# Kernel tuning notes

Hardware: AMD Instinct MI355X
Metric: run time of the kernel (lower is better)

The kernel has to match this reference:

```python
import jax, jax.numpy as jnp
import numpy as np

B, N, F, H, OUT = 64, 512, 128, 256, 6


def setup_inputs() -> dict:
    key = jax.random.key(0)
    ks = jax.random.split(key, 20)
    s = 0.02
    inp = {
        "x": jax.random.normal(ks[0], (B * N, F), dtype=jnp.float32),
        "edge_index": jax.random.randint(ks[1], (2, 16), 0, B * N),
        "edge_weight": jax.random.uniform(ks[2], (16,), dtype=jnp.float32),
        "batch": jnp.repeat(jnp.arange(B, dtype=jnp.int64), N),
        "sigma": jax.random.uniform(ks[3], (1,), dtype=jnp.float32),
        "Wg": s * jax.random.normal(ks[4], (F, F)), "bg": jnp.zeros((F,)),
        "Wrel0": s * jax.random.normal(ks[5], (F, H)), "Wroot0": s * jax.random.normal(ks[6], (F, H)), "brel0": jnp.zeros((H,)),
        "Wrel1": s * jax.random.normal(ks[7], (H, H)), "Wroot1": s * jax.random.normal(ks[8], (H, H)), "brel1": jnp.zeros((H,)),
        "Wrel2": s * jax.random.normal(ks[9], (H, H)), "Wroot2": s * jax.random.normal(ks[10], (H, H)), "brel2": jnp.zeros((H,)),
        "W1": s * jax.random.normal(ks[11], (H, H)), "b1": jnp.zeros((H,)),
        "Wout": s * jax.random.normal(ks[12], (H, OUT)), "bout": jnp.zeros((OUT,)),
    }
    return inp


def _forward(x, sigma, Wg, bg, Wrel0, Wroot0, brel0, Wrel1, Wroot1, brel1,
             Wrel2, Wroot2, brel2, W1, b1, Wout, bout):
    # gdmLinear
    h = x @ Wg + bg                      # [B*N, F]
    hw = h.reshape(B, N, -1)             # to_dense_batch (equal-size windows)
    # pairwise squared distances per window -> Gaussian kernel
    sq = jnp.sum(hw * hw, axis=-1)       # [B, N]
    dist = jnp.maximum(sq[:, :, None] + sq[:, None, :]
                       - 2.0 * jnp.einsum('bnf,bmf->bnm', hw, hw), 0.0)
    A = jnp.exp(-dist / (2.0 * sigma[0] ** 2))   # [B, N, N], all > 0
    A = A * (1.0 - jnp.eye(N, dtype=A.dtype))    # nonzero extraction drops self-loops

    def conv(h, Wrel, Wroot, brel):
        # GraphConv: out_i = W_rel @ sum_j A[j,i] * h_j + b_rel + W_root @ h_i
        agg = jnp.einsum('bji,bjf->bif', A, h)
        return agg @ Wrel + brel + h @ Wroot

    h = hw
    h = jax.nn.relu(conv(h, Wrel0, Wroot0, brel0))
    h = jax.nn.relu(conv(h, Wrel1, Wroot1, brel1))
    h = conv(h, Wrel2, Wroot2, brel2)
    g = jnp.mean(h, axis=1)              # global_mean_pool (equal-size graphs)
    g = jax.nn.relu(g @ W1 + b1)
    return g @ Wout + bout               # [B, OUT]


def reference(x, edge_index, edge_weight, batch, sigma, Wg, bg,
              Wrel0, Wroot0, brel0, Wrel1, Wroot1, brel1,
              Wrel2, Wroot2, brel2, W1, b1, Wout, bout):
    # edge_index / edge_weight / batch inputs are recomputed internally by GdmGNN
    return _forward(x, sigma, Wg, bg, Wrel0, Wroot0, brel0, Wrel1, Wroot1, brel1,
                    Wrel2, Wroot2, brel2, W1, b1, Wout, bout)
```

## Files before the change

kernel.cpp:

```cpp
#include <hip/hip_runtime.h>
#include <math.h>

#define Bsz 64
#define Nn 512
#define Ff 128
#define Hh 256
#define OUTD 6
#define MTOT (Bsz * Nn)

typedef __bf16 bf16x8 __attribute__((ext_vector_type(8)));
typedef float f32x4 __attribute__((ext_vector_type(4)));
typedef int int4v __attribute__((ext_vector_type(4)));
typedef unsigned short ushort4v __attribute__((ext_vector_type(4)));

__device__ __forceinline__ unsigned short f2bf(float f) {
    unsigned u = __float_as_uint(f);
    u += 0x7FFFu + ((u >> 16) & 1u);
    return (unsigned short)(u >> 16);
}
__device__ __forceinline__ float bf2f(unsigned short s) {
    return __uint_as_float(((unsigned)s) << 16);
}

#define SWZ(r) (((r) ^ ((r) >> 2)) & 3)

__device__ __forceinline__ void async_ld16(const unsigned short* g, unsigned short* l) {
    __builtin_amdgcn_global_load_lds(
        (const __attribute__((address_space(1))) void*)g,
        (__attribute__((address_space(3))) void*)l,
        16, 0, 0);
}

#define LDH 40
#define TSZ (128 * 32)
#define AGP 136
#define AGP1 264

__global__ __launch_bounds__(512) void fused_l0(
    const unsigned short* __restrict__ h0T,
    const unsigned short* __restrict__ Arows,
    const unsigned short* __restrict__ h0b,
    const unsigned short* __restrict__ WrelT0,
    const unsigned short* __restrict__ WrootT0,
    const float* __restrict__ brel0,
    unsigned short* __restrict__ h1b,
    unsigned short* __restrict__ h1T)
{
    int id = blockIdx.x;
    int b = id & 63;
    int nt = id >> 6;
    int n0g = nt * 128;
    long nodeBase = (long)b * Nn + n0g;

    const unsigned short* HT = h0T + (long)b * Ff * Nn;
    const unsigned short* AR = Arows + (long)b * Nn * Nn;

    __shared__ unsigned short SA[2 * TSZ];
    __shared__ unsigned short SB[2 * TSZ];
    __shared__ unsigned short aggL[128 * AGP];

    int tid = threadIdx.x;
    int lane = tid & 63;
    int wave = tid >> 6;
    int quad = lane >> 4, l16 = lane & 15;
    int wm = (wave >> 1) * 32, wn = (wave & 1) * 64;
    int sr = lane >> 2, sc = lane & 3;

    {
        f32x4 acc[2][4] = {};
        auto issue = [&](int g) {
            int kk = g << 5;
            unsigned short* Ad = SA + (g & 1) * TSZ;
            unsigned short* Bd = SB + (g & 1) * TSZ;
            int r = wave * 16 + sr;
            int c = sc ^ SWZ(r);
            async_ld16(HT + (long)r * Nn + kk + c * 8, Ad + (wave * 16) * 32);
            async_ld16(AR + (long)(n0g + r) * Nn + kk + c * 8, Bd + (wave * 16) * 32);
        };
        issue(0);
        for (int g = 0; g < (Nn >> 5); ++g) {
            __syncthreads();
            if (g + 1 < (Nn >> 5)) issue(g + 1);
            const unsigned short* Ab = SA + (g & 1) * TSZ;
            const unsigned short* Bb = SB + (g & 1) * TSZ;
            bf16x8 af[2], bfr[4];
            #pragma unroll
            for (int i = 0; i < 2; ++i) {
                int r = wm + i * 16 + l16;
                af[i] = *(const bf16x8*)&Ab[r * 32 + (quad ^ SWZ(r)) * 8];
            }
            #pragma unroll
            for (int j = 0; j < 4; ++j) {
                int r = wn + j * 16 + l16;
                bfr[j] = *(const bf16x8*)&Bb[r * 32 + (quad ^ SWZ(r)) * 8];
            }
            #pragma unroll
            for (int i = 0; i < 2; ++i)
                #pragma unroll
                for (int j = 0; j < 4; ++j)
                    acc[i][j] = __builtin_amdgcn_mfma_f32_16x16x32_bf16(
                        af[i], bfr[j], acc[i][j], 0, 0, 0);
        }
        #pragma unroll
        for (int i = 0; i < 2; ++i) {
            int f = wm + i * 16 + quad * 4;
            #pragma unroll
            for (int j = 0; j < 4; ++j) {
                int nl = wn + j * 16 + l16;
                f32x4 v = acc[i][j];
                ushort4v p;
                p[0] = f2bf(v[0]); p[1] = f2bf(v[1]);
                p[2] = f2bf(v[2]); p[3] = f2bf(v[3]);
                *(ushort4v*)&aggL[nl * AGP + f] = p;
            }
        }
    }
    __syncthreads();

    for (int half = 0; half < 2; ++half) {
        int m0 = half * 128;
        f32x4 acc[2][4] = {};
        auto issue = [&](int g) {
            unsigned short* Ad = SA + (g & 1) * TSZ;
            int r = wave * 16 + sr;
            int c = sc ^ SWZ(r);
            if (g < 4) {
                async_ld16(WrelT0 + (long)(m0 + r) * Ff + (g << 5) + c * 8,
                           Ad + (wave * 16) * 32);
            } else {
                async_ld16(WrootT0 + (long)(m0 + r) * Ff + ((g - 4) << 5) + c * 8,
                           Ad + (wave * 16) * 32);
                unsigned short* Bd = SB + (g & 1) * TSZ;
                async_ld16(h0b + (nodeBase + r) * Ff + ((g - 4) << 5) + c * 8,
                           Bd + (wave * 16) * 32);
            }
        };
        issue(0);
        for (int g = 0; g < 8; ++g) {
            __syncthreads();
            if (g + 1 < 8) issue(g + 1);
            const unsigned short* Ab = SA + (g & 1) * TSZ;
            bf16x8 af[2], bfr[4];
            #pragma unroll
            for (int i = 0; i < 2; ++i) {
                int r = wm + i * 16 + l16;
                af[i] = *(const bf16x8*)&Ab[r * 32 + (quad ^ SWZ(r)) * 8];
            }
            if (g < 4) {
                #pragma unroll
                for (int j = 0; j < 4; ++j) {
                    int nl = wn + j * 16 + l16;
                    bfr[j] = *(const bf16x8*)&aggL[nl * AGP + (g << 5) + quad * 8];
                }
            } else {
                const unsigned short* Bb = SB + (g & 1) * TSZ;
                #pragma unroll
                for (int j = 0; j < 4; ++j) {
                    int r = wn + j * 16 + l16;
                    bfr[j] = *(const bf16x8*)&Bb[r * 32 + (quad ^ SWZ(r)) * 8];
                }
            }
            #pragma unroll
            for (int i = 0; i < 2; ++i)
                #pragma unroll
                for (int j = 0; j < 4; ++j)
                    acc[i][j] = __builtin_amdgcn_mfma_f32_16x16x32_bf16(
                        af[i], bfr[j], acc[i][j], 0, 0, 0);
        }
        #pragma unroll
        for (int i = 0; i < 2; ++i) {
            int of = m0 + wm + i * 16 + quad * 4;
            float b0 = brel0[of + 0], b1 = brel0[of + 1];
            float b2 = brel0[of + 2], b3 = brel0[of + 3];
            #pragma unroll
            for (int j = 0; j < 4; ++j) {
                int nl = wn + j * 16 + l16;
                f32x4 v = acc[i][j];
                float o0 = fmaxf(v[0] + b0, 0.f), o1 = fmaxf(v[1] + b1, 0.f);
                float o2 = fmaxf(v[2] + b2, 0.f), o3 = fmaxf(v[3] + b3, 0.f);
                ushort4v p;
                p[0] = f2bf(o0); p[1] = f2bf(o1); p[2] = f2bf(o2); p[3] = f2bf(o3);
                *(ushort4v*)&h1b[(nodeBase + nl) * Hh + of] = p;
                long base = ((long)b * Hh) * 512 + n0g + nl;
                h1T[base + (long)(of + 0) * 512] = p[0];
                h1T[base + (long)(of + 1) * 512] = p[1];
                h1T[base + (long)(of + 2) * 512] = p[2];
                h1T[base + (long)(of + 3) * 512] = p[3];
            }
        }
    }
}

__global__ __launch_bounds__(512) void fused_l1(
    const unsigned short* __restrict__ h1T,
    const unsigned short* __restrict__ Arows,
    const unsigned short* __restrict__ h1b,
    const unsigned short* __restrict__ WrelT1,
    const unsigned short* __restrict__ WrootT1,
    const float* __restrict__ brel1,
    const float* __restrict__ w,
    float* __restrict__ vpart, float* __restrict__ mpart)
{
    constexpr int ATS = 256 * 32;
    constexpr int BTS = 64 * 32;

    int id = blockIdx.x;
    int b = id & 63;
    int nt = id >> 6;
    int n0g = nt * 64;
    long nodeBase = (long)b * Nn + n0g;

    const unsigned short* HT = h1T + (long)b * Hh * Nn;
    const unsigned short* AR = Arows + (long)b * Nn * Nn;

    __shared__ unsigned short SA[2 * ATS];
    __shared__ unsigned short SB[2 * BTS];
    __shared__ unsigned short aggL[64 * AGP1];

    int tid = threadIdx.x;
    int lane = tid & 63;
    int wave = tid >> 6;
    int quad = lane >> 4, l16 = lane & 15;
    int wm = wave * 32;
    int sr = lane >> 2, sc = lane & 3;

    {
        f32x4 acc[2][4] = {};
        auto issue = [&](int g) {
            int kk = g << 5;
            unsigned short* Ad = SA + (g & 1) * ATS;
            int r = wave * 16 + sr;
            int c = sc ^ SWZ(r);
            async_ld16(HT + (long)r * Nn + kk + c * 8, Ad + (wave * 16) * 32);
            int r2 = 128 + r;
            int c2 = sc ^ SWZ(r2);
            async_ld16(HT + (long)r2 * Nn + kk + c2 * 8, Ad + (128 + wave * 16) * 32);
            if (wave < 4) {
                unsigned short* Bd = SB + (g & 1) * BTS;
                async_ld16(AR + (long)(n0g + r) * Nn + kk + c * 8,
                           Bd + (wave * 16) * 32);
            }
        };
        issue(0);
        for (int g = 0; g < 16; ++g) {
            __syncthreads();
            if (g + 1 < 16) issue(g + 1);
            const unsigned short* Ab = SA + (g & 1) * ATS;
            const unsigned short* Bb = SB + (g & 1) * BTS;
            bf16x8 af[2], bfr[4];
            #pragma unroll
            for (int i = 0; i < 2; ++i) {
                int r = wm + i * 16 + l16;
                af[i] = *(const bf16x8*)&Ab[r * 32 + (quad ^ SWZ(r)) * 8];
            }
            #pragma unroll
            for (int j = 0; j < 4; ++j) {
                int r = j * 16 + l16;
                bfr[j] = *(const bf16x8*)&Bb[r * 32 + (quad ^ SWZ(r)) * 8];
            }
            #pragma unroll
            for (int i = 0; i < 2; ++i)
                #pragma unroll
                for (int j = 0; j < 4; ++j)
                    acc[i][j] = __builtin_amdgcn_mfma_f32_16x16x32_bf16(
                        af[i], bfr[j], acc[i][j], 0, 0, 0);
        }
        #pragma unroll
        for (int i = 0; i < 2; ++i) {
            int f = wm + i * 16 + quad * 4;
            #pragma unroll
            for (int j = 0; j < 4; ++j) {
                int nl = j * 16 + l16;
                f32x4 v = acc[i][j];
                ushort4v p;
                p[0] = f2bf(v[0]); p[1] = f2bf(v[1]);
                p[2] = f2bf(v[2]); p[3] = f2bf(v[3]);
                *(ushort4v*)&aggL[nl * AGP1 + f] = p;
            }
        }
    }
    __syncthreads();

    f32x4 acc[2][4] = {};
    auto issue2 = [&](int g) {
        const unsigned short* Wp = (g < 8) ? WrelT1 : WrootT1;
        int kk = (g & 7) << 5;
        unsigned short* Ad = SA + (g & 1) * ATS;
        int r = wave * 16 + sr;
        int c = sc ^ SWZ(r);
        async_ld16(Wp + (long)r * Hh + kk + c * 8, Ad + (wave * 16) * 32);
        int r2 = 128 + r;
        int c2 = sc ^ SWZ(r2);
        async_ld16(Wp + (long)r2 * Hh + kk + c2 * 8, Ad + (128 + wave * 16) * 32);
        if (g >= 8 && wave < 4) {
            unsigned short* Bd = SB + (g & 1) * BTS;
            async_ld16(h1b + (nodeBase + r) * Hh + kk + c * 8, Bd + (wave * 16) * 32);
        }
    };
    issue2(0);
    for (int g = 0; g < 16; ++g) {
        __syncthreads();
        if (g + 1 < 16) issue2(g + 1);
        const unsigned short* Ab = SA + (g & 1) * ATS;
        bf16x8 af[2], bfr[4];
        #pragma unroll
        for (int i = 0; i < 2; ++i) {
            int r = wm + i * 16 + l16;
            af[i] = *(const bf16x8*)&Ab[r * 32 + (quad ^ SWZ(r)) * 8];
        }
        if (g < 8) {
            #pragma unroll
            for (int j = 0; j < 4; ++j) {
                int nl = j * 16 + l16;
                bfr[j] = *(const bf16x8*)&aggL[nl * AGP1 + (g << 5) + quad * 8];
            }
        } else {
            const unsigned short* Bb = SB + (g & 1) * BTS;
            #pragma unroll
            for (int j = 0; j < 4; ++j) {
                int r = j * 16 + l16;
                bfr[j] = *(const bf16x8*)&Bb[r * 32 + (quad ^ SWZ(r)) * 8];
            }
        }
        #pragma unroll
        for (int i = 0; i < 2; ++i)
            #pragma unroll
            for (int j = 0; j < 4; ++j)
                acc[i][j] = __builtin_amdgcn_mfma_f32_16x16x32_bf16(
                    af[i], bfr[j], acc[i][j], 0, 0, 0);
    }

    #pragma unroll
    for (int i = 0; i < 2; ++i) {
        int lf = wm + i * 16 + quad * 4;
        float b0 = brel1[lf + 0], b1 = brel1[lf + 1];
        float b2 = brel1[lf + 2], b3 = brel1[lf + 3];
        float vp0 = 0.f, vp1 = 0.f, vp2 = 0.f, vp3 = 0.f;
        float mp0 = 0.f, mp1 = 0.f, mp2 = 0.f, mp3 = 0.f;
        #pragma unroll
        for (int j = 0; j < 4; ++j) {
            long node = nodeBase + j * 16 + l16;
            f32x4 v = acc[i][j];
            float o0 = fmaxf(v[0] + b0, 0.f), o1 = fmaxf(v[1] + b1, 0.f);
            float o2 = fmaxf(v[2] + b2, 0.f), o3 = fmaxf(v[3] + b3, 0.f);
            float h0v = bf2f(f2bf(o0)), h1v = bf2f(f2bf(o1));
            float h2v = bf2f(f2bf(o2)), h3v = bf2f(f2bf(o3));
            float wv = w[node];
            vp0 += wv * h0v; vp1 += wv * h1v; vp2 += wv * h2v; vp3 += wv * h3v;
            mp0 += h0v; mp1 += h1v; mp2 += h2v; mp3 += h3v;
        }
        #pragma unroll
        for (int m = 1; m < 16; m <<= 1) {
            vp0 += __shfl_xor(vp0, m); vp1 += __shfl_xor(vp1, m);
            vp2 += __shfl_xor(vp2, m); vp3 += __shfl_xor(vp3, m);
            mp0 += __shfl_xor(mp0, m); mp1 += __shfl_xor(mp1, m);
            mp2 += __shfl_xor(mp2, m); mp3 += __shfl_xor(mp3, m);
        }
        if (l16 == 0) {
            long o = ((long)(b * 8 + nt)) * Hh + lf;
            float4 vv = {vp0, vp1, vp2, vp3};
            float4 mm = {mp0, mp1, mp2, mp3};
            *(float4*)&vpart[o] = vv;
            *(float4*)&mpart[o] = mm;
        }
    }
}

__global__ __launch_bounds__(256) void prep_h0(
    const float* __restrict__ x, const float* __restrict__ Wg,
    const float* __restrict__ bg,
    const float* __restrict__ Wrel0, const float* __restrict__ Wroot0,
    const float* __restrict__ Wrel1, const float* __restrict__ Wroot1,
    unsigned short* __restrict__ T0, unsigned short* __restrict__ T1,
    unsigned short* __restrict__ T2, unsigned short* __restrict__ T3,
    float* __restrict__ w,
    unsigned short* __restrict__ h0b, unsigned short* __restrict__ h0T,
    float* __restrict__ sqv)
{
    if (blockIdx.x < 896) {
        int idx = blockIdx.x * 256 + threadIdx.x;
        if (idx >= 196608) { w[idx - 196608] = 0.f; return; }
        const float* src; unsigned short* dst; int kin; int e;
        if      (idx <  32768) { src = Wrel0;  dst = T0; kin = 128; e = idx; }
        else if (idx <  65536) { src = Wroot0; dst = T1; kin = 128; e = idx - 32768; }
        else if (idx < 131072) { src = Wrel1;  dst = T2; kin = 256; e = idx - 65536; }
        else                   { src = Wroot1; dst = T3; kin = 256; e = idx - 131072; }
        int o = (kin == 128) ? (e >> 7) : (e >> 8);
        int i = e & (kin - 1);
        dst[e] = f2bf(src[(long)i * 256 + o]);
        return;
    }

    __shared__ unsigned short As[128 * LDH];
    __shared__ unsigned short Bs[128 * LDH];
    __shared__ float rsq[128];

    int tid = threadIdx.x;
    int lane = tid & 63;
    int wave = tid >> 6;
    int quad = lane >> 4, l16 = lane & 15;
    int wm = (wave >> 1) * 64, wn = (wave & 1) * 64;
    int m0 = (blockIdx.x - 896) * 128;

    f32x4 acc[4][4] = {};

    for (int k0 = 0; k0 < Ff; k0 += 32) {
        __syncthreads();
        #pragma unroll
        for (int l = 0; l < 2; ++l) {
            int idx = tid + l * 256;
            int r = idx >> 2, ch = idx & 3;
            const float* px = x + (long)(m0 + r) * Ff + k0 + ch * 8;
            float4 xa = *(const float4*)px;
            float4 xb = *(const float4*)(px + 4);
            ushort4v pa, pb;
            pa[0] = f2bf(xa.x); pa[1] = f2bf(xa.y); pa[2] = f2bf(xa.z); pa[3] = f2bf(xa.w);
            pb[0] = f2bf(xb.x); pb[1] = f2bf(xb.y); pb[2] = f2bf(xb.z); pb[3] = f2bf(xb.w);
            *(ushort4v*)&As[r * LDH + ch * 8] = pa;
            *(ushort4v*)&As[r * LDH + ch * 8 + 4] = pb;
            int kk = k0 + ch * 8;
            ushort4v qa, qb;
            #pragma unroll
            for (int u = 0; u < 4; ++u) qa[u] = f2bf(Wg[(long)(kk + u) * 128 + r]);
            #pragma unroll
            for (int u = 0; u < 4; ++u) qb[u] = f2bf(Wg[(long)(kk + 4 + u) * 128 + r]);
            *(ushort4v*)&Bs[r * LDH + ch * 8] = qa;
            *(ushort4v*)&Bs[r * LDH + ch * 8 + 4] = qb;
        }
        __syncthreads();
        bf16x8 af[4], bfr[4];
        #pragma unroll
        for (int i = 0; i < 4; ++i)
            af[i] = *(const bf16x8*)&As[(wm + i * 16 + l16) * LDH + quad * 8];
        #pragma unroll
        for (int j = 0; j < 4; ++j)
            bfr[j] = *(const bf16x8*)&Bs[(wn + j * 16 + l16) * LDH + quad * 8];
        #pragma unroll
        for (int i = 0; i < 4; ++i)
            #pragma unroll
            for (int j = 0; j < 4; ++j)
                acc[i][j] = __builtin_amdgcn_mfma_f32_16x16x32_bf16(
                    af[i], bfr[j], acc[i][j], 0, 0, 0);
    }

    if (tid < 128) rsq[tid] = 0.f;
    __syncthreads();

    #pragma unroll
    for (int i = 0; i < 4; ++i) {
        int lrow = wm + i * 16 + quad * 4;
        int mb = m0 + lrow;
        float rp0 = 0.f, rp1 = 0.f, rp2 = 0.f, rp3 = 0.f;
        #pragma unroll
        for (int j = 0; j < 4; ++j) {
            int n = wn + j * 16 + l16;
            f32x4 v = acc[i][j];
            float bv = bg[n];
            unsigned short s0 = f2bf(v[0] + bv), s1 = f2bf(v[1] + bv);
            unsigned short s2 = f2bf(v[2] + bv), s3 = f2bf(v[3] + bv);
            h0b[(long)(mb + 0) * Ff + n] = s0;
            h0b[(long)(mb + 1) * Ff + n] = s1;
            h0b[(long)(mb + 2) * Ff + n] = s2;
            h0b[(long)(mb + 3) * Ff + n] = s3;
            ushort4v p; p[0] = s0; p[1] = s1; p[2] = s2; p[3] = s3;
            long ti = ((long)(mb >> 9) * Ff + n) * 512 + (mb & 511);
            *(ushort4v*)&h0T[ti] = p;
            float f0 = bf2f(s0), f1 = bf2f(s1), f2 = bf2f(s2), f3 = bf2f(s3);
            rp0 += f0 * f0; rp1 += f1 * f1; rp2 += f2 * f2; rp3 += f3 * f3;
        }
        #pragma unroll
        for (int m = 1; m < 16; m <<= 1) {
            rp0 += __shfl_xor(rp0, m);
            rp1 += __shfl_xor(rp1, m);
            rp2 += __shfl_xor(rp2, m);
            rp3 += __shfl_xor(rp3, m);
        }
        if (l16 == 0) {
            atomicAdd(&rsq[lrow + 0], rp0);
            atomicAdd(&rsq[lrow + 1], rp1);
            atomicAdd(&rsq[lrow + 2], rp2);
            atomicAdd(&rsq[lrow + 3], rp3);
        }
    }
    __syncthreads();
    if (tid < 128) sqv[m0 + tid] = rsq[tid];
}

__global__ __launch_bounds__(512) void gram_A_mfma(
    const unsigned short* __restrict__ h0b, const float* __restrict__ sqv,
    const float* __restrict__ sigma, unsigned short* __restrict__ Aout,
    float* __restrict__ w)
{
    int id = blockIdx.x;
    int b = id & 63;
    int t = id >> 6;
    int i0 = (t & 3) * 128, j0 = (t >> 2) * 128;

    const unsigned short* H = h0b + (long)b * Nn * Ff;
    const float* SQ = sqv + (long)b * Nn;
    unsigned short* Ab = Aout + (long)b * Nn * Nn;

    __shared__ unsigned short Is[2 * TSZ];
    __shared__ unsigned short Js[2 * TSZ];
    __shared__ float rsum[128];

    int tid = threadIdx.x;
    int lane = tid & 63;
    int wave = tid >> 6;
    int quad = lane >> 4, l16 = lane & 15;
    int wm = (wave >> 1) * 32, wn = (wave & 1) * 64;

    int sr = lane >> 2, sc = lane & 3;

    f32x4 acc[2][4] = {};

    auto issue = [&](int g) {
        int kk = g << 5;
        unsigned short* Id = Is + (g & 1) * TSZ;
        unsigned short* Jd = Js + (g & 1) * TSZ;
        int r = wave * 16 + sr;
        int c = sc ^ SWZ(r);
        async_ld16(H + (long)(i0 + r) * Ff + kk + c * 8, Id + (wave * 16) * 32);
        async_ld16(H + (long)(j0 + r) * Ff + kk + c * 8, Jd + (wave * 16) * 32);
    };

    issue(0);
    for (int g = 0; g < (Ff >> 5); ++g) {
        __syncthreads();
        if (g + 1 < (Ff >> 5)) issue(g + 1);
        const unsigned short* Ib = Is + (g & 1) * TSZ;
        const unsigned short* Jb = Js + (g & 1) * TSZ;
        bf16x8 af[2], bfr[4];
        #pragma unroll
        for (int i = 0; i < 2; ++i) {
            int r = wm + i * 16 + l16;
            af[i] = *(const bf16x8*)&Ib[r * 32 + (quad ^ SWZ(r)) * 8];
        }
        #pragma unroll
        for (int j = 0; j < 4; ++j) {
            int r = wn + j * 16 + l16;
            bfr[j] = *(const bf16x8*)&Jb[r * 32 + (quad ^ SWZ(r)) * 8];
        }
        #pragma unroll
        for (int i = 0; i < 2; ++i)
            #pragma unroll
            for (int j = 0; j < 4; ++j)
                acc[i][j] = __builtin_amdgcn_mfma_f32_16x16x32_bf16(
                    af[i], bfr[j], acc[i][j], 0, 0, 0);
    }

    if (tid < 128) rsum[tid] = 0.f;
    __syncthreads();

    float s = sigma[0];
    float inv2s2 = 1.0f / (2.0f * s * s);
    #pragma unroll
    for (int i = 0; i < 2; ++i) {
        int lrow = wm + i * 16 + quad * 4;
        int rb = i0 + lrow;
        float rs0 = 0.f, rs1 = 0.f, rs2 = 0.f, rs3 = 0.f;
        #pragma unroll
        for (int j = 0; j < 4; ++j) {
            int c = j0 + wn + j * 16 + l16;
            float sqc = SQ[c];
            f32x4 v = acc[i][j];
            ushort4v pk;
            float av[4];
            #pragma unroll
            for (int r4 = 0; r4 < 4; ++r4) {
                int r = rb + r4;
                float d = fmaxf(SQ[r] + sqc - 2.0f * v[r4], 0.0f);
                unsigned short a = (r == c) ? (unsigned short)0
                                            : f2bf(__expf(-d * inv2s2));
                pk[r4] = a;
                av[r4] = bf2f(a);
            }
            *(ushort4v*)&Ab[(long)c * Nn + rb] = pk;
            rs0 += av[0]; rs1 += av[1]; rs2 += av[2]; rs3 += av[3];
        }
        #pragma unroll
        for (int m = 1; m < 16; m <<= 1) {
            rs0 += __shfl_xor(rs0, m);
            rs1 += __shfl_xor(rs1, m);
            rs2 += __shfl_xor(rs2, m);
            rs3 += __shfl_xor(rs3, m);
        }
        if (l16 == 0) {
            atomicAdd(&rsum[lrow + 0], rs0);
            atomicAdd(&rsum[lrow + 1], rs1);
            atomicAdd(&rsum[lrow + 2], rs2);
            atomicAdd(&rsum[lrow + 3], rs3);
        }
    }
    __syncthreads();
    if (tid < 128) atomicAdd(&w[(long)b * Nn + i0 + tid], rsum[tid]);
}

__global__ __launch_bounds__(256) void head_kernel(
    const float* __restrict__ vpart, const float* __restrict__ mpart,
    const float* __restrict__ Wrel2, const float* __restrict__ Wroot2,
    const float* __restrict__ brel2,
    const float* __restrict__ W1, const float* __restrict__ b1,
    const float* __restrict__ Wout, const float* __restrict__ bout,
    float* __restrict__ out)
{
    int b = blockIdx.x;
    int j = threadIdx.x;
    __shared__ float vs[Hh], ms[Hh], gs[Hh], g2[Hh];
    float vp = 0.f, mp = 0.f;
    #pragma unroll
    for (int p = 0; p < 8; ++p) {
        long o = ((long)(b * 8 + p)) * Hh + j;
        vp += vpart[o];
        mp += mpart[o];
    }
    vs[j] = vp * (1.0f / (float)Nn);
    ms[j] = mp * (1.0f / (float)Nn);
    __syncthreads();
    float s = brel2[j];
    for (int c = 0; c < Hh; ++c)
        s += vs[c] * Wrel2[c * Hh + j] + ms[c] * Wroot2[c * Hh + j];
    gs[j] = s;
    __syncthreads();
    float t = b1[j];
    for (int k = 0; k < Hh; ++k) t += gs[k] * W1[k * Hh + j];
    g2[j] = fmaxf(t, 0.f);
    __syncthreads();
    if (j < OUTD) {
        float s2 = bout[j];
        for (int k = 0; k < Hh; ++k) s2 += g2[k] * Wout[k * OUTD + j];
        out[b * OUTD + j] = s2;
    }
}

extern "C" void kernel_launch(void* const* d_in, const int* in_sizes, int n_in,
                              void* d_out, int out_size, void* d_ws, size_t ws_size,
                              hipStream_t stream) {
    const float* x      = (const float*)d_in[0];
    const float* sigma  = (const float*)d_in[4];
    const float* Wg     = (const float*)d_in[5];
    const float* bg     = (const float*)d_in[6];
    const float* Wrel0  = (const float*)d_in[7];
    const float* Wroot0 = (const float*)d_in[8];
    const float* brel0  = (const float*)d_in[9];
    const float* Wrel1  = (const float*)d_in[10];
    const float* Wroot1 = (const float*)d_in[11];
    const float* brel1  = (const float*)d_in[12];
    const float* Wrel2  = (const float*)d_in[13];
    const float* Wroot2 = (const float*)d_in[14];
    const float* brel2  = (const float*)d_in[15];
    const float* W1     = (const float*)d_in[16];
    const float* b1     = (const float*)d_in[17];
    const float* Wout   = (const float*)d_in[18];
    const float* bout   = (const float*)d_in[19];
    float* out = (float*)d_out;

    char* ws = (char*)d_ws;
    unsigned short* h0b  = (unsigned short*)(ws + 16777216);
    unsigned short* h0T  = (unsigned short*)(ws + 25165824);
    float*          sq   = (float*)(ws + 33554432);
    unsigned short* Aadj = (unsigned short*)(ws + 33685504);
    unsigned short* h1b  = (unsigned short*)(ws + 84017152);
    unsigned short* h1T  = (unsigned short*)(ws + 100794368);
    unsigned short* WrelT0  = (unsigned short*)(ws + 167903232);
    unsigned short* WrootT0 = (unsigned short*)(ws + 167968768);
    unsigned short* WrelT1  = (unsigned short*)(ws + 168034304);
    unsigned short* WrootT1 = (unsigned short*)(ws + 168165376);
    float*          w     = (float*)(ws + 168558592);
    float*          vpart = (float*)(ws + 168689664);
    float*          mpart = (float*)(ws + 169213952);

    prep_h0<<<1152, 256, 0, stream>>>(x, Wg, bg, Wrel0, Wroot0, Wrel1, Wroot1,
                                      WrelT0, WrootT0, WrelT1, WrootT1,
                                      w, h0b, h0T, sq);

    gram_A_mfma<<<dim3(16 * Bsz, 1, 1), 512, 0, stream>>>(h0b, sq, sigma, Aadj, w);

    fused_l0<<<dim3(4 * Bsz, 1, 1), 512, 0, stream>>>(
        h0T, Aadj, h0b, WrelT0, WrootT0, brel0, h1b, h1T);

    fused_l1<<<dim3(8 * Bsz, 1, 1), 512, 0, stream>>>(
        h1T, Aadj, h1b, WrelT1, WrootT1, brel1, w, vpart, mpart);

    head_kernel<<<Bsz, 256, 0, stream>>>(vpart, mpart, Wrel2, Wroot2, brel2,
                                         W1, b1, Wout, bout, out);
}
```

Baseline: 213.4 us.

## Recompute Gaussian adjacency on the fly inside conv kernels instead of materializing it

Removes the separate gram/adjacency kernel and its 32MB bf16 A matrix in global memory. Both fused layer kernels now recompute the Gram tile from h0b, apply the exp kernel into shared memory, and aggregate immediately. The row-sum weights w are computed per block in shared memory. Layer 0 moves to 64-node tiles so each block covers a full 256-wide output. This trades HBM traffic and one launch for doing the Gram and exp work twice.

```diff
diff --git a/kernel.cpp b/kernel.cpp
--- a/kernel.cpp
+++ b/kernel.cpp
@@ -32,16 +32,18 @@
 }
 
 #define LDH 40
-#define TSZ (128 * 32)
+#define ATS (256 * 32)
+#define BTS (64 * 32)
+#define AJ  136
 #define AGP 136
 #define AGP1 264
 
 __global__ __launch_bounds__(512) void fused_l0(
     const unsigned short* __restrict__ h0T,
-    const unsigned short* __restrict__ Arows,
     const unsigned short* __restrict__ h0b,
     const unsigned short* __restrict__ WrelT0,
     const unsigned short* __restrict__ WrootT0,
+    const float* __restrict__ sqv, const float* __restrict__ sigma,
     const float* __restrict__ brel0,
     unsigned short* __restrict__ h1b,
     unsigned short* __restrict__ h1T)
@@ -49,303 +51,377 @@
     int id = blockIdx.x;
     int b = id & 63;
     int nt = id >> 6;
-    int n0g = nt * 128;
+    int n0g = nt * 64;
     long nodeBase = (long)b * Nn + n0g;
 
-    const unsigned short* HT = h0T + (long)b * Ff * Nn;
-    const unsigned short* AR = Arows + (long)b * Nn * Nn;
-
-    __shared__ unsigned short SA[2 * TSZ];
-    __shared__ unsigned short SB[2 * TSZ];
-    __shared__ unsigned short aggL[128 * AGP];
+    const float* SQ = sqv + (long)b * Nn;
+
+    __shared__ unsigned short SA[2 * ATS];
+    __shared__ unsigned short SB[2 * BTS];
+    __shared__ unsigned short AL[64 * AJ];
 
     int tid = threadIdx.x;
     int lane = tid & 63;
     int wave = tid >> 6;
     int quad = lane >> 4, l16 = lane & 15;
-    int wm = (wave >> 1) * 32, wn = (wave & 1) * 64;
     int sr = lane >> 2, sc = lane & 3;
 
-    {
-        f32x4 acc[2][4] = {};
-        auto issue = [&](int g) {
-            int kk = g << 5;
-            unsigned short* Ad = SA + (g & 1) * TSZ;
-            unsigned short* Bd = SB + (g & 1) * TSZ;
+    float s = sigma[0];
+    float inv2s2 = 1.0f / (2.0f * s * s);
+
+    f32x4 agg[4] = {};
+
+    for (int jt = 0; jt < 4; ++jt) {
+        auto issueG = [&](int ss) {
+            unsigned short* d = SA + (ss & 1) * ATS;
             int r = wave * 16 + sr;
             int c = sc ^ SWZ(r);
-            async_ld16(HT + (long)r * Nn + kk + c * 8, Ad + (wave * 16) * 32);
-            async_ld16(AR + (long)(n0g + r) * Nn + kk + c * 8, Bd + (wave * 16) * 32);
+            async_ld16(h0b + ((long)b * Nn + jt * 128 + r) * Ff + ss * 32 + c * 8,
+                       d + (wave * 16) * 32);
+            if (wave < 4)
+                async_ld16(h0b + (nodeBase + r) * Ff + ss * 32 + c * 8,
+                           d + (128 + wave * 16) * 32);
         };
-        issue(0);
-        for (int g = 0; g < (Nn >> 5); ++g) {
+        f32x4 gacc[4] = {};
+        issueG(0);
+        for (int ss = 0; ss < 4; ++ss) {
             __syncthreads();
-            if (g + 1 < (Nn >> 5)) issue(g + 1);
-            const unsigned short* Ab = SA + (g & 1) * TSZ;
-            const unsigned short* Bb = SB + (g & 1) * TSZ;
-            bf16x8 af[2], bfr[4];
-            #pragma unroll
-            for (int i = 0; i < 2; ++i) {
-                int r = wm + i * 16 + l16;
-                af[i] = *(const bf16x8*)&Ab[r * 32 + (quad ^ SWZ(r)) * 8];
-            }
-            #pragma unroll
-            for (int j = 0; j < 4; ++j) {
-                int r = wn + j * 16 + l16;
-                bfr[j] = *(const bf16x8*)&Bb[r * 32 + (quad ^ SWZ(r)) * 8];
-            }
-            #pragma unroll
-            for (int i = 0; i < 2; ++i)
-                #pragma unroll
-                for (int j = 0; j < 4; ++j)
-                    acc[i][j] = __builtin_amdgcn_mfma_f32_16x16x32_bf16(
-                        af[i], bfr[j], acc[i][j], 0, 0, 0);
-        }
-        #pragma unroll
-        for (int i = 0; i < 2; ++i) {
-            int f = wm + i * 16 + quad * 4;
-            #pragma unroll
-            for (int j = 0; j < 4; ++j) {
-                int nl = wn + j * 16 + l16;
-                f32x4 v = acc[i][j];
-                ushort4v p;
-                p[0] = f2bf(v[0]); p[1] = f2bf(v[1]);
-                p[2] = f2bf(v[2]); p[3] = f2bf(v[3]);
-                *(ushort4v*)&aggL[nl * AGP + f] = p;
-            }
-        }
-    }
-    __syncthreads();
-
-    for (int half = 0; half < 2; ++half) {
-        int m0 = half * 128;
-        f32x4 acc[2][4] = {};
-        auto issue = [&](int g) {
-            unsigned short* Ad = SA + (g & 1) * TSZ;
+            if (ss < 3) issueG(ss + 1);
+            const unsigned short* Sg = SA + (ss & 1) * ATS;
+            int jrow = wave * 16 + l16;
+            bf16x8 af = *(const bf16x8*)&Sg[jrow * 32 + (quad ^ SWZ(jrow)) * 8];
+            #pragma unroll
+            for (int jj = 0; jj < 4; ++jj) {
+                int irow = jj * 16 + l16;
+                bf16x8 bf = *(const bf16x8*)&Sg[(128 + irow) * 32 + (quad ^ SWZ(irow)) * 8];
+                gacc[jj] = __builtin_amdgcn_mfma_f32_16x16x32_bf16(af, bf, gacc[jj], 0, 0, 0);
+            }
+        }
+        int jlb = wave * 16 + quad * 4;
+        #pragma unroll
+        for (int jj = 0; jj < 4; ++jj) {
+            int il = jj * 16 + l16;
+            int iG = n0g + il;
+            float sqi = SQ[iG];
+            f32x4 v = gacc[jj];
+            ushort4v pk;
+            #pragma unroll
+            for (int r4 = 0; r4 < 4; ++r4) {
+                int jG = jt * 128 + jlb + r4;
+                float d = fmaxf(SQ[jG] + sqi - 2.0f * v[r4], 0.0f);
+                pk[r4] = (jG == iG) ? (unsigned short)0 : f2bf(__expf(-d * inv2s2));
+            }
+            *(ushort4v*)&AL[il * AJ + jlb] = pk;
+        }
+        __syncthreads();
+
+        auto issueA = [&](int ss) {
+            unsigned short* d = SA + (ss & 1) * ATS;
             int r = wave * 16 + sr;
             int c = sc ^ SWZ(r);
-            if (g < 4) {
-                async_ld16(WrelT0 + (long)(m0 + r) * Ff + (g << 5) + c * 8,
-                           Ad + (wave * 16) * 32);
-            } else {
-                async_ld16(WrootT0 + (long)(m0 + r) * Ff + ((g - 4) << 5) + c * 8,
-                           Ad + (wave * 16) * 32);
-                unsigned short* Bd = SB + (g & 1) * TSZ;
-                async_ld16(h0b + (nodeBase + r) * Ff + ((g - 4) << 5) + c * 8,
-                           Bd + (wave * 16) * 32);
-            }
+            async_ld16(h0T + ((long)b * Ff + r) * Nn + jt * 128 + ss * 32 + c * 8,
+                       d + (wave * 16) * 32);
         };
-        issue(0);
-        for (int g = 0; g < 8; ++g) {
+        issueA(0);
+        for (int ss = 0; ss < 4; ++ss) {
             __syncthreads();
-            if (g + 1 < 8) issue(g + 1);
-            const unsigned short* Ab = SA + (g & 1) * TSZ;
-            bf16x8 af[2], bfr[4];
-            #pragma unroll
-            for (int i = 0; i < 2; ++i) {
-                int r = wm + i * 16 + l16;
-                af[i] = *(const bf16x8*)&Ab[r * 32 + (quad ^ SWZ(r)) * 8];
-            }
-            if (g < 4) {
-                #pragma unroll
-                for (int j = 0; j < 4; ++j) {
-                    int nl = wn + j * 16 + l16;
-                    bfr[j] = *(const bf16x8*)&aggL[nl * AGP + (g << 5) + quad * 8];
-                }
-            } else {
-                const unsigned short* Bb = SB + (g & 1) * TSZ;
-                #pragma unroll
-                for (int j = 0; j < 4; ++j) {
-                    int r = wn + j * 16 + l16;
-                    bfr[j] = *(const bf16x8*)&Bb[r * 32 + (quad ^ SWZ(r)) * 8];
-                }
-            }
-            #pragma unroll
-            for (int i = 0; i < 2; ++i)
-                #pragma unroll
-                for (int j = 0; j < 4; ++j)
-                    acc[i][j] = __builtin_amdgcn_mfma_f32_16x16x32_bf16(
-                        af[i], bfr[j], acc[i][j], 0, 0, 0);
-        }
+            if (ss < 3) issueA(ss + 1);
+            const unsigned short* Sg = SA + (ss & 1) * ATS;
+            int frow = wave * 16 + l16;
+            bf16x8 af = *(const bf16x8*)&Sg[frow * 32 + (quad ^ SWZ(frow)) * 8];
+            #pragma unroll
+            for (int jj = 0; jj < 4; ++jj) {
+                int il = jj * 16 + l16;
+                bf16x8 bf = *(const bf16x8*)&AL[il * AJ + ss * 32 + quad * 8];
+                agg[jj] = __builtin_amdgcn_mfma_f32_16x16x32_bf16(af, bf, agg[jj], 0, 0, 0);
+            }
+        }
+        __syncthreads();
+    }
+
+    {
+        int fb = wave * 16 + quad * 4;
+        #pragma unroll
+        for (int jj = 0; jj < 4; ++jj) {
+            int il = jj * 16 + l16;
+            f32x4 v = agg[jj];
+            ushort4v p;
+            p[0] = f2bf(v[0]); p[1] = f2bf(v[1]); p[2] = f2bf(v[2]); p[3] = f2bf(v[3]);
+            *(ushort4v*)&AL[il * AGP + fb] = p;
+        }
+    }
+    __syncthreads();
+
+    f32x4 acc2[2][4] = {};
+    auto issue2 = [&](int g) {
+        const unsigned short* Wp = (g < 4) ? WrelT0 : WrootT0;
+        int kk = (g & 3) << 5;
+        unsigned short* d = SA + (g & 1) * ATS;
+        int r = wave * 16 + sr;
+        int c = sc ^ SWZ(r);
+        async_ld16(Wp + (long)r * Ff + kk + c * 8, d + (wave * 16) * 32);
+        int r2 = 128 + r;
+        int c2 = sc ^ SWZ(r2);
+        async_ld16(Wp + (long)r2 * Ff + kk + c2 * 8, d + (128 + wave * 16) * 32);
+        if (g >= 4 && wave < 4)
+            async_ld16(h0b + (nodeBase + r) * Ff + kk + c * 8,
+                       SB + (g & 1) * BTS + (wave * 16) * 32);
+    };
+    issue2(0);
+    for (int g = 0; g < 8; ++g) {
+        __syncthreads();
+        if (g < 7) issue2(g + 1);
+        const unsigned short* Sg = SA + (g & 1) * ATS;
+        bf16x8 af[2], bfr[4];
         #pragma unroll
         for (int i = 0; i < 2; ++i) {
-            int of = m0 + wm + i * 16 + quad * 4;
-            float b0 = brel0[of + 0], b1 = brel0[of + 1];
-            float b2 = brel0[of + 2], b3 = brel0[of + 3];
-            #pragma unroll
-            for (int j = 0; j < 4; ++j) {
-                int nl = wn + j * 16 + l16;
-                f32x4 v = acc[i][j];
-                float o0 = fmaxf(v[0] + b0, 0.f), o1 = fmaxf(v[1] + b1, 0.f);
-                float o2 = fmaxf(v[2] + b2, 0.f), o3 = fmaxf(v[3] + b3, 0.f);
-                ushort4v p;
-                p[0] = f2bf(o0); p[1] = f2bf(o1); p[2] = f2bf(o2); p[3] = f2bf(o3);
-                *(ushort4v*)&h1b[(nodeBase + nl) * Hh + of] = p;
-                long base = ((long)b * Hh) * 512 + n0g + nl;
-                h1T[base + (long)(of + 0) * 512] = p[0];
-                h1T[base + (long)(of + 1) * 512] = p[1];
-                h1T[base + (long)(of + 2) * 512] = p[2];
-                h1T[base + (long)(of + 3) * 512] = p[3];
-            }
+            int row = wave * 32 + i * 16 + l16;
+            af[i] = *(const bf16x8*)&Sg[row * 32 + (quad ^ SWZ(row)) * 8];
+        }
+        if (g < 4) {
+            #pragma unroll
+            for (int jj = 0; jj < 4; ++jj) {
+                int il = jj * 16 + l16;
+                bfr[jj] = *(const bf16x8*)&AL[il * AGP + (g << 5) + quad * 8];
+            }
+        } else {
+            const unsigned short* Bb = SB + (g & 1) * BTS;
+            #pragma unroll
+            for (int jj = 0; jj < 4; ++jj) {
+                int irow = jj * 16 + l16;
+                bfr[jj] = *(const bf16x8*)&Bb[irow * 32 + (quad ^ SWZ(irow)) * 8];
+            }
+        }
+        #pragma unroll
+        for (int i = 0; i < 2; ++i)
+            #pragma unroll
+            for (int jj = 0; jj < 4; ++jj)
+                acc2[i][jj] = __builtin_amdgcn_mfma_f32_16x16x32_bf16(
+                    af[i], bfr[jj], acc2[i][jj], 0, 0, 0);
+    }
+    #pragma unroll
+    for (int i = 0; i < 2; ++i) {
+        int of = wave * 32 + i * 16 + quad * 4;
+        float b0 = brel0[of + 0], b1 = brel0[of + 1];
+        float b2 = brel0[of + 2], b3 = brel0[of + 3];
+        #pragma unroll
+        for (int jj = 0; jj < 4; ++jj) {
+            int nl = jj * 16 + l16;
+            f32x4 v = acc2[i][jj];
+            float o0 = fmaxf(v[0] + b0, 0.f), o1 = fmaxf(v[1] + b1, 0.f);
+            float o2 = fmaxf(v[2] + b2, 0.f), o3 = fmaxf(v[3] + b3, 0.f);
+            ushort4v p;
+            p[0] = f2bf(o0); p[1] = f2bf(o1); p[2] = f2bf(o2); p[3] = f2bf(o3);
+            *(ushort4v*)&h1b[(nodeBase + nl) * Hh + of] = p;
+            long base = ((long)b * Hh) * 512 + n0g + nl;
+            h1T[base + (long)(of + 0) * 512] = p[0];
+            h1T[base + (long)(of + 1) * 512] = p[1];
+            h1T[base + (long)(of + 2) * 512] = p[2];
+            h1T[base + (long)(of + 3) * 512] = p[3];
         }
     }
 }
 
 __global__ __launch_bounds__(512) void fused_l1(
     const unsigned short* __restrict__ h1T,
-    const unsigned short* __restrict__ Arows,
+    const unsigned short* __restrict__ h0b,
     const unsigned short* __restrict__ h1b,
     const unsigned short* __restrict__ WrelT1,
     const unsigned short* __restrict__ WrootT1,
+    const float* __restrict__ sqv, const float* __restrict__ sigma,
     const float* __restrict__ brel1,
-    const float* __restrict__ w,
     float* __restrict__ vpart, float* __restrict__ mpart)
 {
-    constexpr int ATS = 256 * 32;
-    constexpr int BTS = 64 * 32;
-
     int id = blockIdx.x;
     int b = id & 63;
     int nt = id >> 6;
     int n0g = nt * 64;
     long nodeBase = (long)b * Nn + n0g;
 
-    const unsigned short* HT = h1T + (long)b * Hh * Nn;
-    const unsigned short* AR = Arows + (long)b * Nn * Nn;
+    const float* SQ = sqv + (long)b * Nn;
 
     __shared__ unsigned short SA[2 * ATS];
     __shared__ unsigned short SB[2 * BTS];
-    __shared__ unsigned short aggL[64 * AGP1];
+    __shared__ unsigned short AL[64 * AGP1];
+    __shared__ float wloc[64];
 
     int tid = threadIdx.x;
     int lane = tid & 63;
     int wave = tid >> 6;
     int quad = lane >> 4, l16 = lane & 15;
-    int wm = wave * 32;
     int sr = lane >> 2, sc = lane & 3;
 
-    {
-        f32x4 acc[2][4] = {};
-        auto issue = [&](int g) {
-            int kk = g << 5;
-            unsigned short* Ad = SA + (g & 1) * ATS;
+    if (tid < 64) wloc[tid] = 0.f;
+
+    float s = sigma[0];
+    float inv2s2 = 1.0f / (2.0f * s * s);
+
+    f32x4 agg[2][4] = {};
+
+    for (int jt = 0; jt < 4; ++jt) {
+        auto issueG = [&](int ss) {
+            unsigned short* d = SA + (ss & 1) * ATS;
             int r = wave * 16 + sr;
             int c = sc ^ SWZ(r);
-            async_ld16(HT + (long)r * Nn + kk + c * 8, Ad + (wave * 16) * 32);
+            async_ld16(h0b + ((long)b * Nn + jt * 128 + r) * Ff + ss * 32 + c * 8,
+                       d + (wave * 16) * 32);
+            if (wave < 4)
+                async_ld16(h0b + (nodeBase + r) * Ff + ss * 32 + c * 8,
+                           d + (128 + wave * 16) * 32);
+        };
+        f32x4 gacc[4] = {};
+        issueG(0);
+        for (int ss = 0; ss < 4; ++ss) {
+            __syncthreads();
+            if (ss < 3) issueG(ss + 1);
+            const unsigned short* Sg = SA + (ss & 1) * ATS;
+            int jrow = wave * 16 + l16;
+            bf16x8 af = *(const bf16x8*)&Sg[jrow * 32 + (quad ^ SWZ(jrow)) * 8];
+            #pragma unroll
+            for (int jj = 0; jj < 4; ++jj) {
+                int irow = jj * 16 + l16;
+                bf16x8 bf = *(const bf16x8*)&Sg[(128 + irow) * 32 + (quad ^ SWZ(irow)) * 8];
+                gacc[jj] = __builtin_amdgcn_mfma_f32_16x16x32_bf16(af, bf, gacc[jj], 0, 0, 0);
+            }
+        }
+        int jlb = wave * 16 + quad * 4;
+        #pragma unroll
+        for (int jj = 0; jj < 4; ++jj) {
+            int il = jj * 16 + l16;
+            int iG = n0g + il;
+            float sqi = SQ[iG];
+            f32x4 v = gacc[jj];
+            ushort4v pk;
+            float cw = 0.f;
+            #pragma unroll
+            for (int r4 = 0; r4 < 4; ++r4) {
+                int jG = jt * 128 + jlb + r4;
+                float d = fmaxf(SQ[jG] + sqi - 2.0f * v[r4], 0.0f);
+                unsigned short a = (jG == iG) ? (unsigned short)0
+                                              : f2bf(__expf(-d * inv2s2));
+                pk[r4] = a;
+                cw += bf2f(a);
+            }
+            *(ushort4v*)&AL[il * AJ + jlb] = pk;
+            cw += __shfl_xor(cw, 16);
+            cw += __shfl_xor(cw, 32);
+            if (quad == 0) atomicAdd(&wloc[il], cw);
+        }
+        __syncthreads();
+
+        auto issueA = [&](int ss) {
+            unsigned short* d = SA + (ss & 1) * ATS;
+            int r = wave * 16 + sr;
+            int c = sc ^ SWZ(r);
+            async_ld16(h1T + ((long)b * Hh + r) * Nn + jt * 128 + ss * 32 + c * 8,
+                       d + (wave * 16) * 32);
             int r2 = 128 + r;
             int c2 = sc ^ SWZ(r2);
-            async_ld16(HT + (long)r2 * Nn + kk + c2 * 8, Ad + (128 + wave * 16) * 32);
-            if (wave < 4) {
-                unsigned short* Bd = SB + (g & 1) * BTS;
-                async_ld16(AR + (long)(n0g + r) * Nn + kk + c * 8,
-                           Bd + (wave * 16) * 32);
-            }
+            async_ld16(h1T + ((long)b * Hh + r2) * Nn + jt * 128 + ss * 32 + c2 * 8,
+                       d + (128 + wave * 16) * 32);
         };
-        issue(0);
-        for (int g = 0; g < 16; ++g) {
+        issueA(0);
+        for (int ss = 0; ss < 4; ++ss) {
             __syncthreads();
-            if (g + 1 < 16) issue(g + 1);
-            const unsigned short* Ab = SA + (g & 1) * ATS;
-            const unsigned short* Bb = SB + (g & 1) * BTS;
-            bf16x8 af[2], bfr[4];
+            if (ss < 3) issueA(ss + 1);
+            const unsigned short* Sg = SA + (ss & 1) * ATS;
+            bf16x8 af[2];
             #pragma unroll
             for (int i = 0; i < 2; ++i) {
-                int r = wm + i * 16 + l16;
-                af[i] = *(const bf16x8*)&Ab[r * 32 + (quad ^ SWZ(r)) * 8];
-            }
-            #pragma unroll
-            for (int j = 0; j < 4; ++j) {
-                int r = j * 16 + l16;
-                bfr[j] = *(const bf16x8*)&Bb[r * 32 + (quad ^ SWZ(r)) * 8];
-            }
-            #pragma unroll
-            for (int i = 0; i < 2; ++i)
+                int frow = wave * 32 + i * 16 + l16;
+                af[i] = *(const bf16x8*)&Sg[frow * 32 + (quad ^ SWZ(frow)) * 8];
+            }
+            #pragma unroll
+            for (int jj = 0; jj < 4; ++jj) {
+                int il = jj * 16 + l16;
+                bf16x8 bf = *(const bf16x8*)&AL[il * AJ + ss * 32 + quad * 8];
                 #pragma unroll
-                for (int j = 0; j < 4; ++j)
-                    acc[i][j] = __builtin_amdgcn_mfma_f32_16x16x32_bf16(
-                        af[i], bfr[j], acc[i][j], 0, 0, 0);
-        }
-        #pragma unroll
-        for (int i = 0; i < 2; ++i) {
-            int f = wm + i * 16 + quad * 4;
-            #pragma unroll
-            for (int j = 0; j < 4; ++j) {
-                int nl = j * 16 + l16;
-                f32x4 v = acc[i][j];
-                ushort4v p;
-                p[0] = f2bf(v[0]); p[1] = f2bf(v[1]);
-                p[2] = f2bf(v[2]); p[3] = f2bf(v[3]);
-                *(ushort4v*)&aggL[nl * AGP1 + f] = p;
-            }
+                for (int i = 0; i < 2; ++i)
+                    agg[i][jj] = __builtin_amdgcn_mfma_f32_16x16x32_bf16(
+                        af[i], bf, agg[i][jj], 0, 0, 0);
+            }
+        }
+        __syncthreads();
+    }
+
+    #pragma unroll
+    for (int i = 0; i < 2; ++i) {
+        int fb = wave * 32 + i * 16 + quad * 4;
+        #pragma unroll
+        for (int jj = 0; jj < 4; ++jj) {
+            int il = jj * 16 + l16;
+            f32x4 v = agg[i][jj];
+            ushort4v p;
+            p[0] = f2bf(v[0]); p[1] = f2bf(v[1]); p[2] = f2bf(v[2]); p[3] = f2bf(v[3]);
+            *(ushort4v*)&AL[il * AGP1 + fb] = p;
         }
     }
     __syncthreads();
 
-    f32x4 acc[2][4] = {};
+    f32x4 acc2[2][4] = {};
     auto issue2 = [&](int g) {
         const unsigned short* Wp = (g < 8) ? WrelT1 : WrootT1;
         int kk = (g & 7) << 5;
-        unsigned short* Ad = SA + (g & 1) * ATS;
+        unsigned short* d = SA + (g & 1) * ATS;
         int r = wave * 16 + sr;
         int c = sc ^ SWZ(r);
-        async_ld16(Wp + (long)r * Hh + kk + c * 8, Ad + (wave * 16) * 32);
+        async_ld16(Wp + (long)r * Hh + kk + c * 8, d + (wave * 16) * 32);
         int r2 = 128 + r;
         int c2 = sc ^ SWZ(r2);
-        async_ld16(Wp + (long)r2 * Hh + kk + c2 * 8, Ad + (128 + wave * 16) * 32);
-        if (g >= 8 && wave < 4) {
-            unsigned short* Bd = SB + (g & 1) * BTS;
-            async_ld16(h1b + (nodeBase + r) * Hh + kk + c * 8, Bd + (wave * 16) * 32);
-        }
+        async_ld16(Wp + (long)r2 * Hh + kk + c2 * 8, d + (128 + wave * 16) * 32);
+        if (g >= 8 && wave < 4)
+            async_ld16(h1b + (nodeBase + r) * Hh + kk + c * 8,
+                       SB + (g & 1) * BTS + (wave * 16) * 32);
     };
     issue2(0);
     for (int g = 0; g < 16; ++g) {
         __syncthreads();
-        if (g + 1 < 16) issue2(g + 1);
-        const unsigned short* Ab = SA + (g & 1) * ATS;
+        if (g < 15) issue2(g + 1);
+        const unsigned short* Sg = SA + (g & 1) * ATS;
         bf16x8 af[2], bfr[4];
         #pragma unroll
         for (int i = 0; i < 2; ++i) {
-            int r = wm + i * 16 + l16;
-            af[i] = *(const bf16x8*)&Ab[r * 32 + (quad ^ SWZ(r)) * 8];
+            int row = wave * 32 + i * 16 + l16;
+            af[i] = *(const bf16x8*)&Sg[row * 32 + (quad ^ SWZ(row)) * 8];
         }
         if (g < 8) {
             #pragma unroll
-            for (int j = 0; j < 4; ++j) {
-                int nl = j * 16 + l16;
-                bfr[j] = *(const bf16x8*)&aggL[nl * AGP1 + (g << 5) + quad * 8];
+            for (int jj = 0; jj < 4; ++jj) {
+                int il = jj * 16 + l16;
+                bfr[jj] = *(const bf16x8*)&AL[il * AGP1 + (g << 5) + quad * 8];
             }
         } else {
             const unsigned short* Bb = SB + (g & 1) * BTS;
             #pragma unroll
-            for (int j = 0; j < 4; ++j) {
-                int r = j * 16 + l16;
-                bfr[j] = *(const bf16x8*)&Bb[r * 32 + (quad ^ SWZ(r)) * 8];
+            for (int jj = 0; jj < 4; ++jj) {
+                int irow = jj * 16 + l16;
+                bfr[jj] = *(const bf16x8*)&Bb[irow * 32 + (quad ^ SWZ(irow)) * 8];
             }
         }
         #pragma unroll
         for (int i = 0; i < 2; ++i)
             #pragma unroll
-            for (int j = 0; j < 4; ++j)
-                acc[i][j] = __builtin_amdgcn_mfma_f32_16x16x32_bf16(
-                    af[i], bfr[j], acc[i][j], 0, 0, 0);
+            for (int jj = 0; jj < 4; ++jj)
+                acc2[i][jj] = __builtin_amdgcn_mfma_f32_16x16x32_bf16(
+                    af[i], bfr[jj], acc2[i][jj], 0, 0, 0);
     }
 
     #pragma unroll
     for (int i = 0; i < 2; ++i) {
-        int lf = wm + i * 16 + quad * 4;
+        int lf = wave * 32 + i * 16 + quad * 4;
         float b0 = brel1[lf + 0], b1 = brel1[lf + 1];
         float b2 = brel1[lf + 2], b3 = brel1[lf + 3];
         float vp0 = 0.f, vp1 = 0.f, vp2 = 0.f, vp3 = 0.f;
         float mp0 = 0.f, mp1 = 0.f, mp2 = 0.f, mp3 = 0.f;
         #pragma unroll
-        for (int j = 0; j < 4; ++j) {
-            long node = nodeBase + j * 16 + l16;
-            f32x4 v = acc[i][j];
+        for (int jj = 0; jj < 4; ++jj) {
+            int nl = jj * 16 + l16;
+            f32x4 v = acc2[i][jj];
             float o0 = fmaxf(v[0] + b0, 0.f), o1 = fmaxf(v[1] + b1, 0.f);
             float o2 = fmaxf(v[2] + b2, 0.f), o3 = fmaxf(v[3] + b3, 0.f);
             float h0v = bf2f(f2bf(o0)), h1v = bf2f(f2bf(o1));
             float h2v = bf2f(f2bf(o2)), h3v = bf2f(f2bf(o3));
-            float wv = w[node];
+            float wv = wloc[nl];
             vp0 += wv * h0v; vp1 += wv * h1v; vp2 += wv * h2v; vp3 += wv * h3v;
             mp0 += h0v; mp1 += h1v; mp2 += h2v; mp3 += h3v;
         }
@@ -373,13 +449,11 @@
     const float* __restrict__ Wrel1, const float* __restrict__ Wroot1,
     unsigned short* __restrict__ T0, unsigned short* __restrict__ T1,
     unsigned short* __restrict__ T2, unsigned short* __restrict__ T3,
-    float* __restrict__ w,
     unsigned short* __restrict__ h0b, unsigned short* __restrict__ h0T,
     float* __restrict__ sqv)
 {
-    if (blockIdx.x < 896) {
+    if (blockIdx.x < 768) {
         int idx = blockIdx.x * 256 + threadIdx.x;
-        if (idx >= 196608) { w[idx - 196608] = 0.f; return; }
         const float* src; unsigned short* dst; int kin; int e;
         if      (idx <  32768) { src = Wrel0;  dst = T0; kin = 128; e = idx; }
         else if (idx <  65536) { src = Wroot0; dst = T1; kin = 128; e = idx - 32768; }
@@ -400,7 +474,7 @@
     int wave = tid >> 6;
     int quad = lane >> 4, l16 = lane & 15;
     int wm = (wave >> 1) * 64, wn = (wave & 1) * 64;
-    int m0 = (blockIdx.x - 896) * 128;
+    int m0 = (blockIdx.x - 768) * 128;
 
     f32x4 acc[4][4] = {};
 
@@ -484,116 +558,6 @@
     }
     __syncthreads();
     if (tid < 128) sqv[m0 + tid] = rsq[tid];
-}
-
-__global__ __launch_bounds__(512) void gram_A_mfma(
-    const unsigned short* __restrict__ h0b, const float* __restrict__ sqv,
-    const float* __restrict__ sigma, unsigned short* __restrict__ Aout,
-    float* __restrict__ w)
-{
-    int id = blockIdx.x;
-    int b = id & 63;
-    int t = id >> 6;
-    int i0 = (t & 3) * 128, j0 = (t >> 2) * 128;
-
-    const unsigned short* H = h0b + (long)b * Nn * Ff;
-    const float* SQ = sqv + (long)b * Nn;
-    unsigned short* Ab = Aout + (long)b * Nn * Nn;
-
-    __shared__ unsigned short Is[2 * TSZ];
-    __shared__ unsigned short Js[2 * TSZ];
-    __shared__ float rsum[128];
-
-    int tid = threadIdx.x;
-    int lane = tid & 63;
-    int wave = tid >> 6;
-    int quad = lane >> 4, l16 = lane & 15;
-    int wm = (wave >> 1) * 32, wn = (wave & 1) * 64;
-
-    int sr = lane >> 2, sc = lane & 3;
-
-    f32x4 acc[2][4] = {};
-
-    auto issue = [&](int g) {
-        int kk = g << 5;
-        unsigned short* Id = Is + (g & 1) * TSZ;
-        unsigned short* Jd = Js + (g & 1) * TSZ;
-        int r = wave * 16 + sr;
-        int c = sc ^ SWZ(r);
-        async_ld16(H + (long)(i0 + r) * Ff + kk + c * 8, Id + (wave * 16) * 32);
-        async_ld16(H + (long)(j0 + r) * Ff + kk + c * 8, Jd + (wave * 16) * 32);
-    };
-
-    issue(0);
-    for (int g = 0; g < (Ff >> 5); ++g) {
-        __syncthreads();
-        if (g + 1 < (Ff >> 5)) issue(g + 1);
-        const unsigned short* Ib = Is + (g & 1) * TSZ;
-        const unsigned short* Jb = Js + (g & 1) * TSZ;
-        bf16x8 af[2], bfr[4];
-        #pragma unroll
-        for (int i = 0; i < 2; ++i) {
-            int r = wm + i * 16 + l16;
-            af[i] = *(const bf16x8*)&Ib[r * 32 + (quad ^ SWZ(r)) * 8];
-        }
-        #pragma unroll
-        for (int j = 0; j < 4; ++j) {
-            int r = wn + j * 16 + l16;
-            bfr[j] = *(const bf16x8*)&Jb[r * 32 + (quad ^ SWZ(r)) * 8];
-        }
-        #pragma unroll
-        for (int i = 0; i < 2; ++i)
-            #pragma unroll
-            for (int j = 0; j < 4; ++j)
-                acc[i][j] = __builtin_amdgcn_mfma_f32_16x16x32_bf16(
-                    af[i], bfr[j], acc[i][j], 0, 0, 0);
-    }
-
-    if (tid < 128) rsum[tid] = 0.f;
-    __syncthreads();
-
-    float s = sigma[0];
-    float inv2s2 = 1.0f / (2.0f * s * s);
-    #pragma unroll
-    for (int i = 0; i < 2; ++i) {
-        int lrow = wm + i * 16 + quad * 4;
-        int rb = i0 + lrow;
-        float rs0 = 0.f, rs1 = 0.f, rs2 = 0.f, rs3 = 0.f;
-        #pragma unroll
-        for (int j = 0; j < 4; ++j) {
-            int c = j0 + wn + j * 16 + l16;
-            float sqc = SQ[c];
-            f32x4 v = acc[i][j];
-            ushort4v pk;
-            float av[4];
-            #pragma unroll
-            for (int r4 = 0; r4 < 4; ++r4) {
-                int r = rb + r4;
-                float d = fmaxf(SQ[r] + sqc - 2.0f * v[r4], 0.0f);
-                unsigned short a = (r == c) ? (unsigned short)0
-                                            : f2bf(__expf(-d * inv2s2));
-                pk[r4] = a;
-                av[r4] = bf2f(a);
-            }
-            *(ushort4v*)&Ab[(long)c * Nn + rb] = pk;
-            rs0 += av[0]; rs1 += av[1]; rs2 += av[2]; rs3 += av[3];
-        }
-        #pragma unroll
-        for (int m = 1; m < 16; m <<= 1) {
-            rs0 += __shfl_xor(rs0, m);
-            rs1 += __shfl_xor(rs1, m);
-            rs2 += __shfl_xor(rs2, m);
-            rs3 += __shfl_xor(rs3, m);
-        }
-        if (l16 == 0) {
-            atomicAdd(&rsum[lrow + 0], rs0);
-            atomicAdd(&rsum[lrow + 1], rs1);
-            atomicAdd(&rsum[lrow + 2], rs2);
-            atomicAdd(&rsum[lrow + 3], rs3);
-        }
-    }
-    __syncthreads();
-    if (tid < 128) atomicAdd(&w[(long)b * Nn + i0 + tid], rsum[tid]);
 }
 
 __global__ __launch_bounds__(256) void head_kernel(
@@ -659,28 +623,24 @@
     unsigned short* h0b  = (unsigned short*)(ws + 16777216);
     unsigned short* h0T  = (unsigned short*)(ws + 25165824);
     float*          sq   = (float*)(ws + 33554432);
-    unsigned short* Aadj = (unsigned short*)(ws + 33685504);
     unsigned short* h1b  = (unsigned short*)(ws + 84017152);
     unsigned short* h1T  = (unsigned short*)(ws + 100794368);
     unsigned short* WrelT0  = (unsigned short*)(ws + 167903232);
     unsigned short* WrootT0 = (unsigned short*)(ws + 167968768);
     unsigned short* WrelT1  = (unsigned short*)(ws + 168034304);
     unsigned short* WrootT1 = (unsigned short*)(ws + 168165376);
-    float*          w     = (float*)(ws + 168558592);
     float*          vpart = (float*)(ws + 168689664);
     float*          mpart = (float*)(ws + 169213952);
 
-    prep_h0<<<1152, 256, 0, stream>>>(x, Wg, bg, Wrel0, Wroot0, Wrel1, Wroot1,
+    prep_h0<<<1024, 256, 0, stream>>>(x, Wg, bg, Wrel0, Wroot0, Wrel1, Wroot1,
                                       WrelT0, WrootT0, WrelT1, WrootT1,
-                                      w, h0b, h0T, sq);
-
-    gram_A_mfma<<<dim3(16 * Bsz, 1, 1), 512, 0, stream>>>(h0b, sq, sigma, Aadj, w);
-
-    fused_l0<<<dim3(4 * Bsz, 1, 1), 512, 0, stream>>>(
-        h0T, Aadj, h0b, WrelT0, WrootT0, brel0, h1b, h1T);
+                                      h0b, h0T, sq);
+
+    fused_l0<<<dim3(8 * Bsz, 1, 1), 512, 0, stream>>>(
+        h0T, h0b, WrelT0, WrootT0, sq, sigma, brel0, h1b, h1T);
 
     fused_l1<<<dim3(8 * Bsz, 1, 1), 512, 0, stream>>>(
-        h1T, Aadj, h1b, WrelT1, WrootT1, brel1, w, vpart, mpart);
+        h1T, h0b, h1b, WrelT1, WrootT1, sq, sigma, brel1, vpart, mpart);
 
     head_kernel<<<Bsz, 256, 0, stream>>>(vpart, mpart, Wrel2, Wroot2, brel2,
                                          W1, b1, Wout, bout, out);
```

After: 223.5 us. 1.05x slower.
